# Kernel tuning notes

Hardware: AMD Instinct MI355X
Metric: run time of the kernel (lower is better)

The kernel has to match this reference:

```python
import jax, jax.numpy as jnp
import numpy as np

N = 8192
D = 512


def setup_inputs() -> dict:
    key = jax.random.key(0)
    ks = jax.random.split(key, 7)
    X = jax.random.normal(ks[0], (N, D), dtype=jnp.float32)
    adj = jax.random.randint(ks[1], (N, N), 0, 2, dtype=jnp.int32)
    # guarantee at least one neighbor per row (self-loop) so softmax is defined
    adj = adj.at[jnp.arange(N), jnp.arange(N)].set(1)
    s = 1.0 / np.sqrt(D)
    Wq = jax.random.normal(ks[2], (D, D), dtype=jnp.float32) * s
    Wk = jax.random.normal(ks[3], (D, D), dtype=jnp.float32) * s
    Wv = jax.random.normal(ks[4], (D, D), dtype=jnp.float32) * s
    Wo = jax.random.normal(ks[5], (D, D), dtype=jnp.float32) * s
    bo = jnp.zeros((D,), dtype=jnp.float32)
    return {"X": X, "adj": adj, "Wq": Wq, "Wk": Wk, "Wv": Wv, "Wo": Wo, "bo": bo}


def reference(X, adj, Wq, Wk, Wv, Wo, bo):
    # torch Linear(no bias): y = x @ W.T
    Q = X @ Wq.T                                  # [N, D]
    K = X @ Wk.T                                  # [N, D]
    V = X @ Wv.T                                  # [N, D]
    scale = 1.0 / jnp.sqrt(jnp.asarray(D, X.dtype))
    scores = jnp.einsum('nd,md->nm', Q, K) * scale  # [N, N]
    scores = jnp.where(adj == 0, -jnp.inf, scores)
    attn = jax.nn.softmax(scores, axis=-1)          # [N, N]
    out = attn @ V                                  # [N, D]
    out = out @ Wo.T + bo                           # [N, D]
    return out
```

## Files before the change

kernel.cpp:

```cpp
#include <hip/hip_runtime.h>

namespace {

constexpr int NR = 8192;
constexpr int DD = 512;
constexpr int NSPLIT = 4;
constexpr int KVLEN = NR / NSPLIT;
constexpr int KT = 32;
constexpr int NT = KVLEN / KT;
constexpr int QB = 64;
constexpr float SCALE = 0.04419417382415922f;

typedef __bf16 bf16x8 __attribute__((ext_vector_type(8)));
typedef __bf16 bf16x4 __attribute__((ext_vector_type(4)));
typedef float  f32x16 __attribute__((ext_vector_type(16)));
typedef float  f32x4  __attribute__((ext_vector_type(4)));

__device__ __forceinline__ f32x16 mfma32(bf16x8 a, bf16x8 b, f32x16 c) {
    return __builtin_amdgcn_mfma_f32_32x32x16_bf16(a, b, c, 0, 0, 0);
}
__device__ __forceinline__ f32x4 mfma16(bf16x8 a, bf16x8 b, f32x4 c) {
    return __builtin_amdgcn_mfma_f32_16x16x32_bf16(a, b, c, 0, 0, 0);
}

typedef const __attribute__((address_space(1))) void g_void;
typedef __attribute__((address_space(3))) void l_void;
__device__ __forceinline__ void lds_dma16(const void* g, void* l) {
    __builtin_amdgcn_global_load_lds((g_void*)g, (l_void*)l, 16, 0, 0);
}

__device__ __forceinline__ size_t kfa(int n, int d) {
    int tile = n >> 5, kv = n & 31;
    int chunk = (d >> 3) ^ (kv & 7);
    return (size_t)tile * 16384 + kv * 512 + chunk * 8 + (d & 7);
}
__device__ __forceinline__ size_t vfa(int n, int d) {
    size_t chunk = (size_t)(((n >> 5) * 4 + (d >> 7)) * 8 +
                            ((d >> 6) & 1) * 4 + ((d >> 5) & 1) * 2 + ((n >> 4) & 1));
    return chunk * 512 + ((((n >> 3) & 1) * 32 + (d & 31)) * 8) + (n & 7);
}

__global__ void __launch_bounds__(256)
cast_kernel(const float* __restrict__ in, __bf16* __restrict__ out, int n8) {
    int i = blockIdx.x * 256 + threadIdx.x;
    if (i >= n8) return;
    const float4* p = (const float4*)(in + (size_t)i * 8);
    float4 v0 = p[0], v1 = p[1];
    bf16x8 o;
    o[0] = (__bf16)v0.x; o[1] = (__bf16)v0.y; o[2] = (__bf16)v0.z; o[3] = (__bf16)v0.w;
    o[4] = (__bf16)v1.x; o[5] = (__bf16)v1.y; o[6] = (__bf16)v1.z; o[7] = (__bf16)v1.w;
    *(bf16x8*)(out + (size_t)i * 8) = o;
}

__global__ void __launch_bounds__(256)
bitpack_kernel(const int* __restrict__ adj, unsigned* __restrict__ abits) {
    const int w = threadIdx.x >> 6, lane = threadIdx.x & 63;
    const int q = blockIdx.x * 4 + w;
    const int* row = adj + (size_t)q * NR;
    unsigned* orow = abits + (size_t)q * 256;
    for (int i = 0; i < 128; ++i) {
        unsigned long long m = __ballot(row[i * 64 + lane] != 0);
        if (lane == 0) { orow[2 * i] = (unsigned)m; orow[2 * i + 1] = (unsigned)(m >> 32); }
    }
}

template<bool FINAL>
__global__ void __launch_bounds__(256, 2)
gemm_kernel(const __bf16* __restrict__ A, const __bf16* __restrict__ B0,
            const __bf16* __restrict__ B1, const __bf16* __restrict__ B2,
            __bf16* __restrict__ C0, __bf16* __restrict__ C1, __bf16* __restrict__ C2,
            const float* __restrict__ bias, float* __restrict__ Cf,
            const float* __restrict__ lsum)
{
    const __bf16* B = B0;
    __bf16* Cb = C0;
    int mode = 0;
    if (!FINAL) {
        if (blockIdx.y == 1)      { B = B1; Cb = C1; mode = 1; }
        else if (blockIdx.y == 2) { B = B2; Cb = C2; }
    }
    __shared__ __bf16 As[128][72];
    __shared__ __bf16 Bs[128][72];
    const int t = threadIdx.x;
    const int w = t >> 6, lane = t & 63, lo = lane & 31, hi = lane >> 5;
    const int wm = w >> 1, wn = w & 1;
    const int bm = (blockIdx.x >> 2) * 128;
    const int bn = (blockIdx.x & 3) * 128;

    f32x16 acc[2][2];
    #pragma unroll
    for (int a = 0; a < 2; ++a)
        #pragma unroll
        for (int b = 0; b < 2; ++b)
            #pragma unroll
            for (int r = 0; r < 16; ++r) acc[a][b][r] = 0.f;

    for (int k0 = 0; k0 < DD; k0 += 64) {
        __syncthreads();
        #pragma unroll
        for (int pp = 0; pp < 2; ++pp) {
            int r = pp * 64 + (t >> 2), c = (t & 3) * 16;
            if (FINAL) {
                int row = bm + r;
                float l0 = lsum[row], l1 = lsum[NR + row],
                      l2 = lsum[2 * NR + row], l3 = lsum[3 * NR + row];
                float Winv = 1.f / (l0 + l1 + l2 + l3);
                float w0 = l0 * Winv, w1 = l1 * Winv, w2 = l2 * Winv, w3 = l3 * Winv;
                const size_t stride = (size_t)NR * DD;
                #pragma unroll
                for (int cc = 0; cc < 2; ++cc) {
                    const size_t base = (size_t)row * DD + k0 + c + cc * 8;
                    bf16x8 o0 = *(const bf16x8*)(A + base);
                    bf16x8 o1 = *(const bf16x8*)(A + stride + base);
                    bf16x8 o2 = *(const bf16x8*)(A + 2 * stride + base);
                    bf16x8 o3 = *(const bf16x8*)(A + 3 * stride + base);
                    bf16x8 om;
                    #pragma unroll
                    for (int e = 0; e < 8; ++e)
                        om[e] = (__bf16)(w0 * (float)o0[e] + w1 * (float)o1[e] +
                                         w2 * (float)o2[e] + w3 * (float)o3[e]);
                    *(bf16x8*)&As[r][c + cc * 8] = om;
                }
            } else {
                *(bf16x8*)&As[r][c]     = *(const bf16x8*)(A + (size_t)(bm + r) * DD + k0 + c);
                *(bf16x8*)&As[r][c + 8] = *(const bf16x8*)(A + (size_t)(bm + r) * DD + k0 + c + 8);
            }
            *(bf16x8*)&Bs[r][c]     = *(const bf16x8*)(B + (size_t)(bn + r) * DD + k0 + c);
            *(bf16x8*)&Bs[r][c + 8] = *(const bf16x8*)(B + (size_t)(bn + r) * DD + k0 + c + 8);
        }
        __syncthreads();
        #pragma unroll
        for (int ks = 0; ks < 4; ++ks) {
            bf16x8 a0 = *(const bf16x8*)&As[wm * 64 + lo][ks * 16 + hi * 8];
            bf16x8 a1 = *(const bf16x8*)&As[wm * 64 + 32 + lo][ks * 16 + hi * 8];
            bf16x8 b0 = *(const bf16x8*)&Bs[wn * 64 + lo][ks * 16 + hi * 8];
            bf16x8 b1 = *(const bf16x8*)&Bs[wn * 64 + 32 + lo][ks * 16 + hi * 8];
            acc[0][0] = mfma32(a0, b0, acc[0][0]);
            acc[0][1] = mfma32(a0, b1, acc[0][1]);
            acc[1][0] = mfma32(a1, b0, acc[1][0]);
            acc[1][1] = mfma32(a1, b1, acc[1][1]);
        }
    }
    #pragma unroll
    for (int mi = 0; mi < 2; ++mi)
        #pragma unroll
        for (int ni = 0; ni < 2; ++ni) {
            int col = bn + wn * 64 + ni * 32 + lo;
            float bv = 0.f;
            if (FINAL) bv = bias[col];
            #pragma unroll
            for (int r = 0; r < 16; ++r) {
                int row = bm + wm * 64 + mi * 32 + (r & 3) + 8 * (r >> 2) + 4 * hi;
                if (FINAL) {
                    Cf[(size_t)row * DD + col] = acc[mi][ni][r] + bv;
                } else {
                    size_t a = (mode == 1) ? kfa(row, col) : ((size_t)row * DD + col);
                    Cb[a] = (__bf16)acc[mi][ni][r];
                }
            }
        }
}

__global__ void __launch_bounds__(256)
repack_v(const __bf16* __restrict__ V, __bf16* __restrict__ VF) {
    __shared__ __bf16 tile[64][72];
    const int t = threadIdx.x;
    const int rb = blockIdx.x * 64;
    const int cb = blockIdx.y * 64;
    #pragma unroll
    for (int pp = 0; pp < 2; ++pp) {
        int r = pp * 32 + (t >> 3), c = (t & 7) * 8;
        *(bf16x8*)&tile[r][c] = *(const bf16x8*)(V + (size_t)(rb + r) * DD + cb + c);
    }
    __syncthreads();
    #pragma unroll
    for (int pp = 0; pp < 2; ++pp) {
        int vid = pp * 256 + t;
        int oct = vid >> 6;
        int dd = vid & 63;
        bf16x8 o;
        #pragma unroll
        for (int e = 0; e < 8; ++e) o[e] = tile[oct * 8 + e][dd];
        *(bf16x8*)(VF + vfa(rb + oct * 8, cb + dd)) = o;
    }
}

__global__ void __launch_bounds__(256, 2)
flash_kernel(const __bf16* __restrict__ Qg, const __bf16* __restrict__ KF,
             const __bf16* __restrict__ VF, const unsigned* __restrict__ abits,
             __bf16* __restrict__ Opart, float* __restrict__ lsum_g)
{
    __shared__ __bf16 Klds[2][16384];
    __shared__ __bf16 Pl[2][QB][40];
    __shared__ float  ll[QB];

    const int t = threadIdx.x;
    const int w = t >> 6, lane = t & 63;
    const int lo = lane & 31, hi = lane >> 5;
    const int l15 = lane & 15, G = lane >> 4;
    const int bid = blockIdx.x;
    const int xcd = bid & 7;
    const int split = xcd >> 1;
    const int qblk = (((xcd & 1) << 6) | (bid >> 3)) * QB;
    const int kv0 = split * KVLEN;
    const int tile0 = kv0 >> 5;

    bf16x8 qa[16];
    #pragma unroll
    for (int ks = 0; ks < 16; ++ks)
        qa[ks] = *(const bf16x8*)(Qg + (size_t)(qblk + w * 16 + l15) * DD + ks * 32 + G * 8);

    f32x16 O[2][2][2];
    #pragma unroll
    for (int h = 0; h < 2; ++h)
        #pragma unroll
        for (int a = 0; a < 2; ++a)
            #pragma unroll
            for (int b = 0; b < 2; ++b)
                #pragma unroll
                for (int r = 0; r < 16; ++r) O[h][a][b][r] = 0.f;

    const unsigned* abp = abits + (size_t)(qblk + w * 16 + l15) * 256 + tile0;
    unsigned wcur = abp[0];
    float l_run = 0.f;
    const int hsw = l15 & 7;

    #pragma unroll
    for (int i = 0; i < 8; ++i)
        lds_dma16(KF + (size_t)tile0 * 16384 + w * 4096 + i * 512 + lane * 8,
                  &Klds[0][w * 4096 + i * 512]);
    asm volatile("s_waitcnt vmcnt(0)" ::: "memory");
    __syncthreads();

    {
        #pragma unroll
        for (int i = 0; i < 8; ++i)
            lds_dma16(KF + (size_t)(tile0 + 1) * 16384 + w * 4096 + i * 512 + lane * 8,
                      &Klds[1][w * 4096 + i * 512]);
        f32x4 St0, St1;
        #pragma unroll
        for (int r = 0; r < 4; ++r) { St0[r] = 0.f; St1[r] = 0.f; }
        #pragma unroll
        for (int ks = 0; ks < 16; ++ks) {
            int csw = (((ks * 4 + G) ^ hsw) << 3);
            bf16x8 k0 = *(const bf16x8*)&Klds[0][l15 * 512 + csw];
            bf16x8 k1 = *(const bf16x8*)&Klds[0][(16 + l15) * 512 + csw];
            St0 = mfma16(k0, qa[ks], St0);
            St1 = mfma16(k1, qa[ks], St1);
        }
        float l_add = 0.f;
        bf16x4 p0v, p1v;
        #pragma unroll
        for (int r = 0; r < 4; ++r) {
            float pv0 = ((wcur >> (G * 4 + r)) & 1u) ? __expf(St0[r] * SCALE) : 0.f;
            float pv1 = ((wcur >> (16 + G * 4 + r)) & 1u) ? __expf(St1[r] * SCALE) : 0.f;
            l_add += pv0 + pv1;
            p0v[r] = (__bf16)pv0; p1v[r] = (__bf16)pv1;
        }
        *(bf16x4*)&Pl[0][w * 16 + l15][G * 4]      = p0v;
        *(bf16x4*)&Pl[0][w * 16 + l15][16 + G * 4] = p1v;
        float a = l_add + __shfl_xor(l_add, 16);
        a += __shfl_xor(a, 32);
        l_run += a;
        unsigned wnxt = abp[1];
        asm volatile("s_waitcnt vmcnt(1) lgkmcnt(0)" ::: "memory");
        asm volatile("s_barrier" ::: "memory");
        wcur = wnxt;
    }

    for (int tl = 1; tl < NT; ++tl) {
        const int b = tl & 1;
        const int tn = (tl + 1 == NT) ? 0 : tl + 1;

        const __bf16* vf = VF + (size_t)((tile0 + tl - 1) * 4 + w) * 4096;
        bf16x8 vb[8];
        #pragma unroll
        for (int i = 0; i < 8; ++i)
            vb[i] = *(const bf16x8*)(vf + i * 512 + lane * 8);
        bf16x8 pa[2][2];
        #pragma unroll
        for (int mi = 0; mi < 2; ++mi)
            #pragma unroll
            for (int ksp = 0; ksp < 2; ++ksp)
                pa[mi][ksp] = *(const bf16x8*)&Pl[b ^ 1][mi * 32 + lo][ksp * 16 + hi * 8];
        #pragma unroll
        for (int i = 0; i < 8; ++i)
            lds_dma16(KF + (size_t)(tile0 + tn) * 16384 + w * 4096 + i * 512 + lane * 8,
                      &Klds[b ^ 1][w * 4096 + i * 512]);

        __builtin_amdgcn_s_setprio(1);
        f32x4 St0, St1;
        #pragma unroll
        for (int r = 0; r < 4; ++r) { St0[r] = 0.f; St1[r] = 0.f; }
        #pragma unroll
        for (int ks = 0; ks < 16; ++ks) {
            int csw = (((ks * 4 + G) ^ hsw) << 3);
            bf16x8 k0 = *(const bf16x8*)&Klds[b][l15 * 512 + csw];
            bf16x8 k1 = *(const bf16x8*)&Klds[b][(16 + l15) * 512 + csw];
            St0 = mfma16(k0, qa[ks], St0);
            St1 = mfma16(k1, qa[ks], St1);
        }
        #pragma unroll
        for (int h = 0; h < 2; ++h)
            #pragma unroll
            for (int ni = 0; ni < 2; ++ni) {
                O[h][0][ni] = mfma32(pa[0][0], vb[h * 4 + ni * 2 + 0], O[h][0][ni]);
                O[h][1][ni] = mfma32(pa[1][0], vb[h * 4 + ni * 2 + 0], O[h][1][ni]);
                O[h][0][ni] = mfma32(pa[0][1], vb[h * 4 + ni * 2 + 1], O[h][0][ni]);
                O[h][1][ni] = mfma32(pa[1][1], vb[h * 4 + ni * 2 + 1], O[h][1][ni]);
            }
        __builtin_amdgcn_s_setprio(0);

        {
            float l_add = 0.f;
            bf16x4 p0v, p1v;
            #pragma unroll
            for (int r = 0; r < 4; ++r) {
                float pv0 = ((wcur >> (G * 4 + r)) & 1u) ? __expf(St0[r] * SCALE) : 0.f;
                float pv1 = ((wcur >> (16 + G * 4 + r)) & 1u) ? __expf(St1[r] * SCALE) : 0.f;
                l_add += pv0 + pv1;
                p0v[r] = (__bf16)pv0; p1v[r] = (__bf16)pv1;
            }
            *(bf16x4*)&Pl[b][w * 16 + l15][G * 4]      = p0v;
            *(bf16x4*)&Pl[b][w * 16 + l15][16 + G * 4] = p1v;
            float a = l_add + __shfl_xor(l_add, 16);
            a += __shfl_xor(a, 32);
            l_run += a;
        }
        unsigned wnxt = abp[tn];
        asm volatile("s_waitcnt vmcnt(1) lgkmcnt(0)" ::: "memory");
        asm volatile("s_barrier" ::: "memory");
        wcur = wnxt;
    }
    {
        const int b = (NT - 1) & 1;
        bf16x8 pa[2][2];
        #pragma unroll
        for (int mi = 0; mi < 2; ++mi)
            #pragma unroll
            for (int ksp = 0; ksp < 2; ++ksp)
                pa[mi][ksp] = *(const bf16x8*)&Pl[b][mi * 32 + lo][ksp * 16 + hi * 8];
        const __bf16* vf = VF + (size_t)((tile0 + NT - 1) * 4 + w) * 4096;
        #pragma unroll
        for (int h = 0; h < 2; ++h)
            #pragma unroll
            for (int ni = 0; ni < 2; ++ni) {
                bf16x8 vb0 = *(const bf16x8*)(vf + (h * 4 + ni * 2 + 0) * 512 + lane * 8);
                bf16x8 vb1 = *(const bf16x8*)(vf + (h * 4 + ni * 2 + 1) * 512 + lane * 8);
                O[h][0][ni] = mfma32(pa[0][0], vb0, O[h][0][ni]);
                O[h][1][ni] = mfma32(pa[1][0], vb0, O[h][1][ni]);
                O[h][0][ni] = mfma32(pa[0][1], vb1, O[h][0][ni]);
                O[h][1][ni] = mfma32(pa[1][1], vb1, O[h][1][ni]);
            }
    }
    if (lane < 16) {
        ll[w * 16 + lane] = l_run;
        lsum_g[(size_t)split * NR + qblk + w * 16 + lane] = l_run;
    }
    __syncthreads();
    #pragma unroll
    for (int mi = 0; mi < 2; ++mi)
        #pragma unroll
        for (int g = 0; g < 4; ++g) {
            float4 lv = *(const float4*)&ll[mi * 32 + 8 * g + 4 * hi];
            #pragma unroll
            for (int j = 0; j < 4; ++j) {
                float lval = (&lv.x)[j];
                float inv = (lval > 0.f) ? 1.f / lval : 0.f;
                int row = qblk + mi * 32 + 8 * g + 4 * hi + j;
                #pragma unroll
                for (int h = 0; h < 2; ++h)
                    #pragma unroll
                    for (int ni = 0; ni < 2; ++ni) {
                        int col = w * 128 + h * 64 + ni * 32 + lo;
                        Opart[(size_t)split * NR * DD + (size_t)row * DD + col] =
                            (__bf16)(O[h][mi][ni][g * 4 + j] * inv);
                    }
            }
        }
}

}

extern "C" void kernel_launch(void* const* d_in, const int* in_sizes, int n_in,
                              void* d_out, int out_size, void* d_ws, size_t ws_size,
                              hipStream_t stream)
{
    (void)in_sizes; (void)n_in; (void)out_size; (void)ws_size;
    const float* X  = (const float*)d_in[0];
    const int*   adj = (const int*)d_in[1];
    const float* Wq = (const float*)d_in[2];
    const float* Wk = (const float*)d_in[3];
    const float* Wv = (const float*)d_in[4];
    const float* Wo = (const float*)d_in[5];
    const float* bo = (const float*)d_in[6];
    float* out = (float*)d_out;

    char* ws = (char*)d_ws;
    __bf16* Xb   = (__bf16*)(ws + 0);
    __bf16* Wqb  = (__bf16*)(ws + 8388608);
    __bf16* Wkb  = (__bf16*)(ws + 8912896);
    __bf16* Wvb  = (__bf16*)(ws + 9437184);
    __bf16* Wob  = (__bf16*)(ws + 9961472);
    __bf16* Qb   = (__bf16*)(ws + 10485760);
    __bf16* KFb  = (__bf16*)(ws + 18874368);
    __bf16* VFb  = (__bf16*)(ws + 27262976);
    unsigned* abits = (unsigned*)(ws + 35651584);
    __bf16* Vb   = (__bf16*)(ws + 44040192);
    __bf16* Op   = (__bf16*)(ws + 44040192);
    float*  lseb = (float*)(ws + 77594624);

    bitpack_kernel<<<2048, 256, 0, stream>>>(adj, abits);
    cast_kernel<<<2048, 256, 0, stream>>>(X,  Xb,  NR * DD / 8);
    cast_kernel<<<128,  256, 0, stream>>>(Wq, Wqb, DD * DD / 8);
    cast_kernel<<<128,  256, 0, stream>>>(Wk, Wkb, DD * DD / 8);
    cast_kernel<<<128,  256, 0, stream>>>(Wv, Wvb, DD * DD / 8);
    cast_kernel<<<128,  256, 0, stream>>>(Wo, Wob, DD * DD / 8);

    gemm_kernel<false><<<dim3(256, 3), 256, 0, stream>>>(Xb, Wqb, Wkb, Wvb,
                                                         Qb, KFb, Vb, nullptr, nullptr, nullptr);
    repack_v<<<dim3(128, 8), 256, 0, stream>>>(Vb, VFb);
    flash_kernel<<<512, 256, 0, stream>>>(Qb, KFb, VFb, abits, Op, lseb);
    gemm_kernel<true><<<dim3(256, 1), 256, 0, stream>>>(Op, Wob, nullptr, nullptr,
                                                        nullptr, nullptr, nullptr, bo, out, lseb);
}
```

Before: 432.4 us.

## Specialize flash kernel warps into QK-softmax producers and PV consumers

The flash kernel now runs 6 waves per block over 32 query rows. Two waves compute QK^T scores and the masked exp, while four waves issue the K-tile DMA and the P·V MFMAs, with one block barrier per tile. The grid doubles to 1024 blocks with 384 threads and three blocks per CU. The aim is to overlap the score/exp phase with the PV accumulation through warp specialization and to raise occupancy. In exchange, each K tile loaded into LDS is now reused by only 32 query rows instead of 64, which doubles K and V traffic per query.

```diff
diff --git a/kernel.cpp b/kernel.cpp
--- a/kernel.cpp
+++ b/kernel.cpp
@@ -8,7 +8,7 @@
 constexpr int KVLEN = NR / NSPLIT;
 constexpr int KT = 32;
 constexpr int NT = KVLEN / KT;
-constexpr int QB = 64;
+constexpr int QB = 32;
 constexpr float SCALE = 0.04419417382415922f;
 
 typedef __bf16 bf16x8 __attribute__((ext_vector_type(8)));
@@ -185,13 +185,13 @@
     }
 }
 
-__global__ void __launch_bounds__(256, 2)
+__global__ void __launch_bounds__(384, 3)
 flash_kernel(const __bf16* __restrict__ Qg, const __bf16* __restrict__ KF,
              const __bf16* __restrict__ VF, const unsigned* __restrict__ abits,
              __bf16* __restrict__ Opart, float* __restrict__ lsum_g)
 {
     __shared__ __bf16 Klds[2][16384];
-    __shared__ __bf16 Pl[2][QB][40];
+    __shared__ __bf16 Pl[2][QB][44];
     __shared__ float  ll[QB];
 
     const int t = threadIdx.x;
@@ -201,117 +201,57 @@
     const int bid = blockIdx.x;
     const int xcd = bid & 7;
     const int split = xcd >> 1;
-    const int qblk = (((xcd & 1) << 6) | (bid >> 3)) * QB;
+    const int qblk = (((xcd & 1) << 7) | (bid >> 3)) * QB;
     const int kv0 = split * KVLEN;
     const int tile0 = kv0 >> 5;
+    const bool isQK = (w < 2);
+    const int pw = w - 2;
 
     bf16x8 qa[16];
-    #pragma unroll
-    for (int ks = 0; ks < 16; ++ks)
-        qa[ks] = *(const bf16x8*)(Qg + (size_t)(qblk + w * 16 + l15) * DD + ks * 32 + G * 8);
-
-    f32x16 O[2][2][2];
-    #pragma unroll
-    for (int h = 0; h < 2; ++h)
-        #pragma unroll
-        for (int a = 0; a < 2; ++a)
-            #pragma unroll
-            for (int b = 0; b < 2; ++b)
-                #pragma unroll
-                for (int r = 0; r < 16; ++r) O[h][a][b][r] = 0.f;
-
-    const unsigned* abp = abits + (size_t)(qblk + w * 16 + l15) * 256 + tile0;
-    unsigned wcur = abp[0];
+    const unsigned* abp = nullptr;
+    unsigned wcur = 0;
     float l_run = 0.f;
     const int hsw = l15 & 7;
-
-    #pragma unroll
-    for (int i = 0; i < 8; ++i)
-        lds_dma16(KF + (size_t)tile0 * 16384 + w * 4096 + i * 512 + lane * 8,
-                  &Klds[0][w * 4096 + i * 512]);
-    asm volatile("s_waitcnt vmcnt(0)" ::: "memory");
+    if (isQK) {
+        #pragma unroll
+        for (int ks = 0; ks < 16; ++ks)
+            qa[ks] = *(const bf16x8*)(Qg + (size_t)(qblk + w * 16 + l15) * DD + ks * 32 + G * 8);
+        abp = abits + (size_t)(qblk + w * 16 + l15) * 256 + tile0;
+        wcur = abp[0];
+    }
+
+    f32x16 O[4];
+    #pragma unroll
+    for (int j = 0; j < 4; ++j)
+        #pragma unroll
+        for (int r = 0; r < 16; ++r) O[j][r] = 0.f;
+
+    if (!isQK) {
+        #pragma unroll
+        for (int i = 0; i < 8; ++i)
+            lds_dma16(KF + (size_t)tile0 * 16384 + pw * 4096 + i * 512 + lane * 8,
+                      &Klds[0][pw * 4096 + i * 512]);
+    }
     __syncthreads();
 
-    {
-        #pragma unroll
-        for (int i = 0; i < 8; ++i)
-            lds_dma16(KF + (size_t)(tile0 + 1) * 16384 + w * 4096 + i * 512 + lane * 8,
-                      &Klds[1][w * 4096 + i * 512]);
-        f32x4 St0, St1;
-        #pragma unroll
-        for (int r = 0; r < 4; ++r) { St0[r] = 0.f; St1[r] = 0.f; }
-        #pragma unroll
-        for (int ks = 0; ks < 16; ++ks) {
-            int csw = (((ks * 4 + G) ^ hsw) << 3);
-            bf16x8 k0 = *(const bf16x8*)&Klds[0][l15 * 512 + csw];
-            bf16x8 k1 = *(const bf16x8*)&Klds[0][(16 + l15) * 512 + csw];
-            St0 = mfma16(k0, qa[ks], St0);
-            St1 = mfma16(k1, qa[ks], St1);
-        }
-        float l_add = 0.f;
-        bf16x4 p0v, p1v;
-        #pragma unroll
-        for (int r = 0; r < 4; ++r) {
-            float pv0 = ((wcur >> (G * 4 + r)) & 1u) ? __expf(St0[r] * SCALE) : 0.f;
-            float pv1 = ((wcur >> (16 + G * 4 + r)) & 1u) ? __expf(St1[r] * SCALE) : 0.f;
-            l_add += pv0 + pv1;
-            p0v[r] = (__bf16)pv0; p1v[r] = (__bf16)pv1;
-        }
-        *(bf16x4*)&Pl[0][w * 16 + l15][G * 4]      = p0v;
-        *(bf16x4*)&Pl[0][w * 16 + l15][16 + G * 4] = p1v;
-        float a = l_add + __shfl_xor(l_add, 16);
-        a += __shfl_xor(a, 32);
-        l_run += a;
-        unsigned wnxt = abp[1];
-        asm volatile("s_waitcnt vmcnt(1) lgkmcnt(0)" ::: "memory");
-        asm volatile("s_barrier" ::: "memory");
-        wcur = wnxt;
-    }
-
-    for (int tl = 1; tl < NT; ++tl) {
+    for (int tl = 0; tl < NT; ++tl) {
         const int b = tl & 1;
         const int tn = (tl + 1 == NT) ? 0 : tl + 1;
-
-        const __bf16* vf = VF + (size_t)((tile0 + tl - 1) * 4 + w) * 4096;
-        bf16x8 vb[8];
-        #pragma unroll
-        for (int i = 0; i < 8; ++i)
-            vb[i] = *(const bf16x8*)(vf + i * 512 + lane * 8);
-        bf16x8 pa[2][2];
-        #pragma unroll
-        for (int mi = 0; mi < 2; ++mi)
-            #pragma unroll
-            for (int ksp = 0; ksp < 2; ++ksp)
-                pa[mi][ksp] = *(const bf16x8*)&Pl[b ^ 1][mi * 32 + lo][ksp * 16 + hi * 8];
-        #pragma unroll
-        for (int i = 0; i < 8; ++i)
-            lds_dma16(KF + (size_t)(tile0 + tn) * 16384 + w * 4096 + i * 512 + lane * 8,
-                      &Klds[b ^ 1][w * 4096 + i * 512]);
-
-        __builtin_amdgcn_s_setprio(1);
-        f32x4 St0, St1;
-        #pragma unroll
-        for (int r = 0; r < 4; ++r) { St0[r] = 0.f; St1[r] = 0.f; }
-        #pragma unroll
-        for (int ks = 0; ks < 16; ++ks) {
-            int csw = (((ks * 4 + G) ^ hsw) << 3);
-            bf16x8 k0 = *(const bf16x8*)&Klds[b][l15 * 512 + csw];
-            bf16x8 k1 = *(const bf16x8*)&Klds[b][(16 + l15) * 512 + csw];
-            St0 = mfma16(k0, qa[ks], St0);
-            St1 = mfma16(k1, qa[ks], St1);
-        }
-        #pragma unroll
-        for (int h = 0; h < 2; ++h)
-            #pragma unroll
-            for (int ni = 0; ni < 2; ++ni) {
-                O[h][0][ni] = mfma32(pa[0][0], vb[h * 4 + ni * 2 + 0], O[h][0][ni]);
-                O[h][1][ni] = mfma32(pa[1][0], vb[h * 4 + ni * 2 + 0], O[h][1][ni]);
-                O[h][0][ni] = mfma32(pa[0][1], vb[h * 4 + ni * 2 + 1], O[h][0][ni]);
-                O[h][1][ni] = mfma32(pa[1][1], vb[h * 4 + ni * 2 + 1], O[h][1][ni]);
-            }
-        __builtin_amdgcn_s_setprio(0);
-
-        {
+        if (isQK) {
+            unsigned wn = abp[tn];
+            f32x4 St0, St1;
+            #pragma unroll
+            for (int r = 0; r < 4; ++r) { St0[r] = 0.f; St1[r] = 0.f; }
+            __builtin_amdgcn_s_setprio(1);
+            #pragma unroll
+            for (int ks = 0; ks < 16; ++ks) {
+                int csw = (((ks * 4 + G) ^ hsw) << 3);
+                bf16x8 k0 = *(const bf16x8*)&Klds[b][l15 * 512 + csw];
+                bf16x8 k1 = *(const bf16x8*)&Klds[b][(16 + l15) * 512 + csw];
+                St0 = mfma16(k0, qa[ks], St0);
+                St1 = mfma16(k1, qa[ks], St1);
+            }
+            __builtin_amdgcn_s_setprio(0);
             float l_add = 0.f;
             bf16x4 p0v, p1v;
             #pragma unroll
@@ -326,58 +266,70 @@
             float a = l_add + __shfl_xor(l_add, 16);
             a += __shfl_xor(a, 32);
             l_run += a;
-        }
-        unsigned wnxt = abp[tn];
-        asm volatile("s_waitcnt vmcnt(1) lgkmcnt(0)" ::: "memory");
-        asm volatile("s_barrier" ::: "memory");
-        wcur = wnxt;
-    }
-    {
-        const int b = (NT - 1) & 1;
-        bf16x8 pa[2][2];
-        #pragma unroll
-        for (int mi = 0; mi < 2; ++mi)
-            #pragma unroll
-            for (int ksp = 0; ksp < 2; ++ksp)
-                pa[mi][ksp] = *(const bf16x8*)&Pl[b][mi * 32 + lo][ksp * 16 + hi * 8];
-        const __bf16* vf = VF + (size_t)((tile0 + NT - 1) * 4 + w) * 4096;
-        #pragma unroll
-        for (int h = 0; h < 2; ++h)
-            #pragma unroll
-            for (int ni = 0; ni < 2; ++ni) {
-                bf16x8 vb0 = *(const bf16x8*)(vf + (h * 4 + ni * 2 + 0) * 512 + lane * 8);
-                bf16x8 vb1 = *(const bf16x8*)(vf + (h * 4 + ni * 2 + 1) * 512 + lane * 8);
-                O[h][0][ni] = mfma32(pa[0][0], vb0, O[h][0][ni]);
-                O[h][1][ni] = mfma32(pa[1][0], vb0, O[h][1][ni]);
-                O[h][0][ni] = mfma32(pa[0][1], vb1, O[h][0][ni]);
-                O[h][1][ni] = mfma32(pa[1][1], vb1, O[h][1][ni]);
-            }
-    }
-    if (lane < 16) {
-        ll[w * 16 + lane] = l_run;
-        lsum_g[(size_t)split * NR + qblk + w * 16 + lane] = l_run;
+            wcur = wn;
+        } else {
+            #pragma unroll
+            for (int i = 0; i < 8; ++i)
+                lds_dma16(KF + (size_t)(tile0 + tn) * 16384 + pw * 4096 + i * 512 + lane * 8,
+                          &Klds[b ^ 1][pw * 4096 + i * 512]);
+            if (tl > 0) {
+                bf16x8 pa0 = *(const bf16x8*)&Pl[b ^ 1][lo][hi * 8];
+                bf16x8 pa1 = *(const bf16x8*)&Pl[b ^ 1][lo][16 + hi * 8];
+                const __bf16* vf = VF + (size_t)((tile0 + tl - 1) * 4 + pw) * 4096;
+                __builtin_amdgcn_s_setprio(1);
+                #pragma unroll
+                for (int jh = 0; jh < 2; ++jh) {
+                    bf16x8 vb0 = *(const bf16x8*)(vf + (jh * 4 + 0) * 512 + lane * 8);
+                    bf16x8 vb1 = *(const bf16x8*)(vf + (jh * 4 + 1) * 512 + lane * 8);
+                    bf16x8 vb2 = *(const bf16x8*)(vf + (jh * 4 + 2) * 512 + lane * 8);
+                    bf16x8 vb3 = *(const bf16x8*)(vf + (jh * 4 + 3) * 512 + lane * 8);
+                    O[jh * 2 + 0] = mfma32(pa0, vb0, O[jh * 2 + 0]);
+                    O[jh * 2 + 0] = mfma32(pa1, vb1, O[jh * 2 + 0]);
+                    O[jh * 2 + 1] = mfma32(pa0, vb2, O[jh * 2 + 1]);
+                    O[jh * 2 + 1] = mfma32(pa1, vb3, O[jh * 2 + 1]);
+                }
+                __builtin_amdgcn_s_setprio(0);
+            }
+        }
+        __syncthreads();
+    }
+    if (isQK) {
+        if (lane < 16) {
+            ll[w * 16 + lane] = l_run;
+            lsum_g[(size_t)split * NR + qblk + w * 16 + lane] = l_run;
+        }
+    } else {
+        const int pb = (NT - 1) & 1;
+        bf16x8 pa0 = *(const bf16x8*)&Pl[pb][lo][hi * 8];
+        bf16x8 pa1 = *(const bf16x8*)&Pl[pb][lo][16 + hi * 8];
+        const __bf16* vf = VF + (size_t)((tile0 + NT - 1) * 4 + pw) * 4096;
+        #pragma unroll
+        for (int j = 0; j < 4; ++j) {
+            bf16x8 vb0 = *(const bf16x8*)(vf + (j * 2 + 0) * 512 + lane * 8);
+            bf16x8 vb1 = *(const bf16x8*)(vf + (j * 2 + 1) * 512 + lane * 8);
+            O[j] = mfma32(pa0, vb0, O[j]);
+            O[j] = mfma32(pa1, vb1, O[j]);
+        }
     }
     __syncthreads();
-    #pragma unroll
-    for (int mi = 0; mi < 2; ++mi)
+    if (!isQK) {
         #pragma unroll
         for (int g = 0; g < 4; ++g) {
-            float4 lv = *(const float4*)&ll[mi * 32 + 8 * g + 4 * hi];
-            #pragma unroll
-            for (int j = 0; j < 4; ++j) {
-                float lval = (&lv.x)[j];
+            float4 lv = *(const float4*)&ll[g * 8 + 4 * hi];
+            #pragma unroll
+            for (int e = 0; e < 4; ++e) {
+                float lval = (&lv.x)[e];
                 float inv = (lval > 0.f) ? 1.f / lval : 0.f;
-                int row = qblk + mi * 32 + 8 * g + 4 * hi + j;
+                int row = qblk + g * 8 + 4 * hi + e;
                 #pragma unroll
-                for (int h = 0; h < 2; ++h)
-                    #pragma unroll
-                    for (int ni = 0; ni < 2; ++ni) {
-                        int col = w * 128 + h * 64 + ni * 32 + lo;
-                        Opart[(size_t)split * NR * DD + (size_t)row * DD + col] =
-                            (__bf16)(O[h][mi][ni][g * 4 + j] * inv);
-                    }
-            }
-        }
+                for (int j = 0; j < 4; ++j) {
+                    int col = pw * 128 + j * 32 + lo;
+                    Opart[(size_t)split * NR * DD + (size_t)row * DD + col] =
+                        (__bf16)(O[j][g * 4 + e] * inv);
+                }
+            }
+        }
+    }
 }
 
 }
@@ -420,7 +372,7 @@
     gemm_kernel<false><<<dim3(256, 3), 256, 0, stream>>>(Xb, Wqb, Wkb, Wvb,
                                                          Qb, KFb, Vb, nullptr, nullptr, nullptr);
     repack_v<<<dim3(128, 8), 256, 0, stream>>>(Vb, VFb);
-    flash_kernel<<<512, 256, 0, stream>>>(Qb, KFb, VFb, abits, Op, lseb);
+    flash_kernel<<<1024, 384, 0, stream>>>(Qb, KFb, VFb, abits, Op, lseb);
     gemm_kernel<true><<<dim3(256, 1), 256, 0, stream>>>(Op, Wob, nullptr, nullptr,
                                                         nullptr, nullptr, nullptr, bo, out, lseb);
 }
```

Result: slower. 1.107 ms (+156.0%).
